# Kernel optimization log

Hardware: AMD Instinct MI355X
Metric: run time of the kernel (lower is better)

The kernel has to match this reference:

```python
import jax, jax.numpy as jnp
import numpy as np

B, S, F, H = 128, 1024, 512, 128


def setup_inputs() -> dict:
    key = jax.random.key(0)
    ks = jax.random.split(key, 12)
    # ragged valid lengths; force one full-length sequence so padded max == S
    lengths = jax.random.randint(ks[0], (B,), S // 4, S + 1)
    lengths = lengths.at[0].set(S)
    mask = (jnp.arange(S)[None, :] < lengths[:, None]).astype(jnp.float32)
    x = jax.random.normal(ks[1], (B, S, F), jnp.float32) * mask[:, :, None]
    s = 1.0 / np.sqrt(H)

    def u(k, shape):
        return jax.random.uniform(k, shape, jnp.float32, -s, s)

    return {
        "x": x,
        "Wp": u(ks[2], (H, F)), "bp": u(ks[3], (H,)),
        "Wih0": u(ks[4], (3 * H, H)), "Whh0": u(ks[5], (3 * H, H)),
        "bih0": u(ks[6], (3 * H,)), "bhh0": u(ks[7], (3 * H,)),
        "Wih1": u(ks[8], (3 * H, H)), "Whh1": u(ks[9], (3 * H, H)),
        "bih1": u(ks[10], (3 * H,)), "bhh1": u(ks[11], (3 * H,)),
    }


def _gru_layer(xs, Wih, Whh, bih, bhh):
    # xs: [S, B, H_in] -> outputs [S, B, H]; torch nn.GRU gate math (r,z,n order)
    xg = jnp.einsum('sbi,gi->sbg', xs, Wih) + bih  # precompute input gates [S,B,3H]
    Hh = Whh.shape[1]

    def step(h, xg_t):
        hg = h @ Whh.T + bhh
        xr, xz, xn = jnp.split(xg_t, 3, axis=-1)
        hr, hz, hn = jnp.split(hg, 3, axis=-1)
        r = jax.nn.sigmoid(xr + hr)
        z = jax.nn.sigmoid(xz + hz)
        n = jnp.tanh(xn + r * hn)
        h_new = (1.0 - z) * n + z * h
        return h_new, h_new

    h0 = jnp.zeros((xs.shape[1], Hh), xs.dtype)
    _, hs = jax.lax.scan(step, h0, xg)
    return hs


def reference(x, Wp, bp, Wih0, Whh0, bih0, bhh0, Wih1, Whh1, bih1, bhh1):
    # valid lengths: rows whose feature-sum is nonzero
    lengths = (jnp.sum(x, axis=-1) != 0).astype(jnp.int32).sum(axis=1)  # [B]
    proj = x @ Wp.T + bp  # [B,S,H]
    # sort by descending length (module returns outputs in SORTED order, no unsort)
    order = jnp.argsort(-lengths)
    sorted_lengths = lengths[order]
    xs = jnp.transpose(proj[order], (1, 0, 2))  # [S,B,H]
    h1 = _gru_layer(xs, Wih0, Whh0, bih0, bhh0)
    h2 = _gru_layer(h1, Wih1, Whh1, bih1, bhh1)
    out = jnp.transpose(h2, (1, 0, 2))  # [B,S,H]
    # pad_packed_sequence zeros outputs beyond each valid length
    valid = (jnp.arange(S)[None, :] < sorted_lengths[:, None]).astype(out.dtype)
    out = out * valid[:, :, None]
    # mean over padded length (max length == S here), zeros included, as in torch
    return out.mean(axis=1)
```

## Files before the change

### kernel.cpp

```cpp
#include <hip/hip_runtime.h>
#include <hip/hip_bf16.h>

#define BB 128
#define SS 1024
#define FF 512
#define HH 128
#define G3 384

typedef __attribute__((ext_vector_type(8))) short bf16x8;
typedef __attribute__((ext_vector_type(4))) float f32x4;
typedef _Float16 half2_t __attribute__((ext_vector_type(2)));

__global__ void zero_len_kernel(int* len) { len[threadIdx.x] = 0; }

__global__ void lengths_kernel(const float* __restrict__ x, int* __restrict__ len) {
    int wave = threadIdx.x >> 6;
    int lane = threadIdx.x & 63;
    long row = (long)blockIdx.x * 4 + wave;
    const float4* p = (const float4*)&x[row * FF + lane * 8];
    float4 v0 = p[0], v1 = p[1];
    float s = v0.x + v0.y + v0.z + v0.w + v1.x + v1.y + v1.z + v1.w;
    #pragma unroll
    for (int off = 32; off > 0; off >>= 1) s += __shfl_down(s, off, 64);
    if (lane == 0 && s != 0.0f) atomicAdd(&len[row >> 10], 1);
}

__global__ void rank_kernel(const int* __restrict__ len, int* __restrict__ rank) {
    int i = threadIdx.x;
    int li = len[i];
    int r = 0;
    for (int jj = 0; jj < BB; jj++) {
        int lj = len[jj];
        if (lj > li || (lj == li && jj < i)) r++;
    }
    rank[i] = r;
}

__device__ __forceinline__ short bf_hi(float w, float& hf) {
    unsigned u = __builtin_bit_cast(unsigned, w);
    unsigned r = (u + 0x7FFFu + ((u >> 16) & 1u)) & 0xFFFF0000u;
    hf = __builtin_bit_cast(float, r);
    return (short)(r >> 16);
}
__device__ __forceinline__ short bf_rn(float w) {
    unsigned u = __builtin_bit_cast(unsigned, w);
    unsigned r = u + 0x7FFFu + ((u >> 16) & 1u);
    return (short)(r >> 16);
}

__global__ __launch_bounds__(256) void gemm_mfma(
    const float* __restrict__ A, const float* __restrict__ W,
    const float* __restrict__ bias, float* __restrict__ C,
    int M, int N, int K)
{
    const int tid  = threadIdx.x;
    const int wvid = tid >> 6;
    const int lane = tid & 63;
    const int m0   = blockIdx.x * 64 + wvid * 16;
    const int n0   = blockIdx.y * 128;
    const int KS   = K >> 5;

    __shared__ __align__(16) short sh[2][8][64][8];

    f32x4 acc[8];
    #pragma unroll
    for (int i = 0; i < 8; i++) acc[i] = (f32x4){0.f, 0.f, 0.f, 0.f};

    const int arow = m0 + (lane & 15);
    const int koff = (lane >> 4) << 3;

    for (int ks = 0; ks < KS; ks++) {
        __syncthreads();
        #pragma unroll
        for (int i = 0; i < 2; i++) {
            int p  = tid + i * 256;
            int nt = p >> 6, ln = p & 63;
            const float* src = &W[(size_t)(n0 + nt * 16 + (ln & 15)) * K
                                  + ks * 32 + ((ln >> 4) << 3)];
            float w8[8];
            *(float4*)&w8[0] = *(const float4*)&src[0];
            *(float4*)&w8[4] = *(const float4*)&src[4];
            short hi8[8], lo8[8];
            #pragma unroll
            for (int e = 0; e < 8; e++) {
                float hf; hi8[e] = bf_hi(w8[e], hf);
                lo8[e] = bf_rn(w8[e] - hf);
            }
            *(bf16x8*)&sh[0][nt][ln][0] = *(bf16x8*)hi8;
            *(bf16x8*)&sh[1][nt][ln][0] = *(bf16x8*)lo8;
        }
        const float* ap = &A[(size_t)arow * K + ks * 32 + koff];
        float av[8];
        *(float4*)&av[0] = *(const float4*)&ap[0];
        *(float4*)&av[4] = *(const float4*)&ap[4];
        short ah[8], al[8];
        #pragma unroll
        for (int e = 0; e < 8; e++) {
            float hf; ah[e] = bf_hi(av[e], hf);
            al[e] = bf_rn(av[e] - hf);
        }
        bf16x8 ahi = *(bf16x8*)ah, alo = *(bf16x8*)al;
        __syncthreads();
        #pragma unroll
        for (int nt = 0; nt < 8; nt++) {
            bf16x8 bhi = *(bf16x8*)&sh[0][nt][lane][0];
            bf16x8 blo = *(bf16x8*)&sh[1][nt][lane][0];
            acc[nt] = __builtin_amdgcn_mfma_f32_16x16x32_bf16(ahi, bhi, acc[nt], 0, 0, 0);
            acc[nt] = __builtin_amdgcn_mfma_f32_16x16x32_bf16(ahi, blo, acc[nt], 0, 0, 0);
            acc[nt] = __builtin_amdgcn_mfma_f32_16x16x32_bf16(alo, bhi, acc[nt], 0, 0, 0);
        }
    }
    const int crow = m0 + ((lane >> 4) << 2);
    const int ccol = n0 + (lane & 15);
    #pragma unroll
    for (int nt = 0; nt < 8; nt++) {
        int col = ccol + nt * 16;
        float bv = bias[col];
        #pragma unroll
        for (int r = 0; r < 4; r++)
            C[(size_t)(crow + r) * N + col] = acc[nt][r] + bv;
    }
}

__device__ __forceinline__ float fast_sigmoid(float x) {
    return __builtin_amdgcn_rcpf(1.0f + __expf(-x));
}
__device__ __forceinline__ float fast_tanh(float x) {
    return 1.0f - 2.0f * __builtin_amdgcn_rcpf(1.0f + __expf(2.0f * x));
}
__device__ __forceinline__ half2_t bc16(unsigned u) {
    return __builtin_bit_cast(half2_t, u);
}
__device__ __forceinline__ unsigned pk16(float x, float y) {
    half2_t h; h[0] = (_Float16)x; h[1] = (_Float16)y;
    return __builtin_bit_cast(unsigned, h);
}
__device__ __forceinline__ float fdot2_(half2_t a, half2_t b, float c) {
#if __has_builtin(__builtin_amdgcn_fdot2)
    return __builtin_amdgcn_fdot2(a, b, c, false);
#else
    return c + (float)a[0] * (float)b[0] + (float)a[1] * (float)b[1];
#endif
}

template<int FINAL>
__global__ __launch_bounds__(512, 1) void gru_rec(
    const float* __restrict__ xg,
    const float* __restrict__ Whh,
    const float* __restrict__ bhh,
    float* __restrict__ h_out,
    const int* __restrict__ len,
    const int* __restrict__ rank)
{
    const int b   = blockIdx.x;
    const int tid = threadIdx.x;
    const int j   = tid >> 2;
    const int kq  = tid & 3;

    __shared__ __align__(16) _Float16 h16[2][HH];
    __shared__ __align__(16) float    h32[2][HH];

    unsigned wv[3][16];
    #pragma unroll
    for (int g = 0; g < 3; g++) {
        const float* wr = &Whh[(size_t)(g * HH + j) * HH + kq * 32];
        #pragma unroll
        for (int m = 0; m < 16; m++) wv[g][m] = pk16(wr[2 * m], wr[2 * m + 1]);
    }

    float b_r = 0.f, b_z = 0.f, b_n = 0.f;
    if (kq == 0) { b_r = bhh[j]; b_z = bhh[HH + j]; b_n = bhh[2 * HH + j]; }
    const float* xgb = xg + (size_t)b * SS * G3;

    if (tid < HH) { h16[0][tid] = (_Float16)0.f; h32[0][tid] = 0.f; }
    float hprev = 0.0f, osum = 0.0f;
    const int L = FINAL ? len[b] : 0;

    float xr = 0.f, xz = 0.f, xn = 0.f;
    if (kq == 0) { xr = xgb[j]; xz = xgb[HH + j]; xn = xgb[2 * HH + j]; }
    __syncthreads();

    for (int t = 0; t < SS; t++) {
        #pragma unroll
        for (int g = 0; g < 3; g++)
            #pragma unroll
            for (int m = 0; m < 16; m += 4)
                asm volatile("" : "+v"(wv[g][m]), "+v"(wv[g][m + 1]),
                                  "+v"(wv[g][m + 2]), "+v"(wv[g][m + 3]));

        if (!FINAL && t > 0 && tid >= 64 && tid < 96) {
            int c = tid - 64;
            float4 hv = ((const float4*)h32[t & 1])[c];
            *(float4*)&h_out[((size_t)b * SS + (t - 1)) * HH + c * 4] = hv;
        }
        float nxr = 0.f, nxz = 0.f, nxn = 0.f;
        if (kq == 0 && t + 1 < SS) {
            const float* p = xgb + (size_t)(t + 1) * G3;
            nxr = p[j]; nxz = p[HH + j]; nxn = p[2 * HH + j];
        }
        const unsigned* hp = (const unsigned*)(&h16[t & 1][0]) + kq * 16;
        float a0 = 0.f, a1 = 0.f, a2 = 0.f;
        float c0 = 0.f, c1 = 0.f, c2 = 0.f;
        #pragma unroll
        for (int i = 0; i < 4; i++) {
            uint4 hv = *(const uint4*)(hp + i * 4);
            half2_t q0 = bc16(hv.x), q1 = bc16(hv.y),
                    q2 = bc16(hv.z), q3 = bc16(hv.w);
            if ((i & 1) == 0) {
                a0 = fdot2_(bc16(wv[0][i * 4 + 0]), q0, a0);
                a0 = fdot2_(bc16(wv[0][i * 4 + 1]), q1, a0);
                a0 = fdot2_(bc16(wv[0][i * 4 + 2]), q2, a0);
                a0 = fdot2_(bc16(wv[0][i * 4 + 3]), q3, a0);
                a1 = fdot2_(bc16(wv[1][i * 4 + 0]), q0, a1);
                a1 = fdot2_(bc16(wv[1][i * 4 + 1]), q1, a1);
                a1 = fdot2_(bc16(wv[1][i * 4 + 2]), q2, a1);
                a1 = fdot2_(bc16(wv[1][i * 4 + 3]), q3, a1);
                a2 = fdot2_(bc16(wv[2][i * 4 + 0]), q0, a2);
                a2 = fdot2_(bc16(wv[2][i * 4 + 1]), q1, a2);
                a2 = fdot2_(bc16(wv[2][i * 4 + 2]), q2, a2);
                a2 = fdot2_(bc16(wv[2][i * 4 + 3]), q3, a2);
            } else {
                c0 = fdot2_(bc16(wv[0][i * 4 + 0]), q0, c0);
                c0 = fdot2_(bc16(wv[0][i * 4 + 1]), q1, c0);
                c0 = fdot2_(bc16(wv[0][i * 4 + 2]), q2, c0);
                c0 = fdot2_(bc16(wv[0][i * 4 + 3]), q3, c0);
                c1 = fdot2_(bc16(wv[1][i * 4 + 0]), q0, c1);
                c1 = fdot2_(bc16(wv[1][i * 4 + 1]), q1, c1);
                c1 = fdot2_(bc16(wv[1][i * 4 + 2]), q2, c1);
                c1 = fdot2_(bc16(wv[1][i * 4 + 3]), q3, c1);
                c2 = fdot2_(bc16(wv[2][i * 4 + 0]), q0, c2);
                c2 = fdot2_(bc16(wv[2][i * 4 + 1]), q1, c2);
                c2 = fdot2_(bc16(wv[2][i * 4 + 2]), q2, c2);
                c2 = fdot2_(bc16(wv[2][i * 4 + 3]), q3, c2);
            }
        }
        float s0 = a0 + c0, s1 = a1 + c1, s2 = a2 + c2;
        s0 += __shfl_xor(s0, 1, 64); s1 += __shfl_xor(s1, 1, 64); s2 += __shfl_xor(s2, 1, 64);
        s0 += __shfl_xor(s0, 2, 64); s1 += __shfl_xor(s1, 2, 64); s2 += __shfl_xor(s2, 2, 64);
        if (kq == 0) {
            float r = fast_sigmoid(xr + s0 + b_r);
            float z = fast_sigmoid(xz + s1 + b_z);
            float n = fast_tanh(xn + r * (s2 + b_n));
            float h = (1.0f - z) * n + z * hprev;
            hprev = h;
            h16[(t + 1) & 1][j] = (_Float16)h;
            h32[(t + 1) & 1][j] = h;
            if (FINAL) { if (t < L) osum += h; }
        }
        xr = nxr; xz = nxz; xn = nxn;
        __syncthreads();
    }
    if (!FINAL && tid >= 64 && tid < 96) {
        int c = tid - 64;
        float4 hv = ((const float4*)h32[SS & 1])[c];
        *(float4*)&h_out[((size_t)b * SS + (SS - 1)) * HH + c * 4] = hv;
    }
    if (FINAL && kq == 0) {
        h_out[(size_t)rank[b] * HH + j] = osum * (1.0f / (float)SS);
    }
}

extern "C" void kernel_launch(void* const* d_in, const int* in_sizes, int n_in,
                              void* d_out, int out_size, void* d_ws, size_t ws_size,
                              hipStream_t stream) {
    const float* x    = (const float*)d_in[0];
    const float* Wp   = (const float*)d_in[1];
    const float* bp   = (const float*)d_in[2];
    const float* Wih0 = (const float*)d_in[3];
    const float* Whh0 = (const float*)d_in[4];
    const float* bih0 = (const float*)d_in[5];
    const float* bhh0 = (const float*)d_in[6];
    const float* Wih1 = (const float*)d_in[7];
    const float* Whh1 = (const float*)d_in[8];
    const float* bih1 = (const float*)d_in[9];
    const float* bhh1 = (const float*)d_in[10];
    float* out = (float*)d_out;

    int* len  = (int*)d_ws;
    int* rank = len + 128;
    float* proj = (float*)((char*)d_ws + 4096);
    float* xgb  = proj + (size_t)BB * SS * HH;

    zero_len_kernel<<<1, 128, 0, stream>>>(len);
    lengths_kernel<<<(BB * SS) / 4, 256, 0, stream>>>(x, len);
    rank_kernel<<<1, 128, 0, stream>>>(len, rank);

    gemm_mfma<<<dim3(BB * SS / 64, 1), 256, 0, stream>>>(x, Wp, bp, proj,
                                                         BB * SS, HH, FF);
    gemm_mfma<<<dim3(BB * SS / 64, 3), 256, 0, stream>>>(proj, Wih0, bih0, xgb,
                                                         BB * SS, G3, HH);
    gru_rec<0><<<BB, 512, 0, stream>>>(xgb, Whh0, bhh0, proj, len, rank);

    gemm_mfma<<<dim3(BB * SS / 64, 3), 256, 0, stream>>>(proj, Wih1, bih1, xgb,
                                                         BB * SS, G3, HH);
    gru_rec<1><<<BB, 512, 0, stream>>>(xgb, Whh1, bhh1, out, len, rank);
}
```

Before: 2.058 ms.

## Store recurrent weights in AGPRs and reduce partial sums with DPP

Moves the 48 packed fp16 weight registers per thread out of VGPRs into accumulation registers, written once and read back with v_accvgpr_read before each dot product. The 4-lane partial-sum reduction now uses DPP quad permutes instead of ds_swizzle/shuffle, and the dot chain is reordered into two interleaved accumulators per gate. The goal is to relieve VGPR pressure and avoid spills at 512 threads per block, and to shorten the cross-lane reduction on the serial per-step path. In exchange, every step adds 48 AGPR read instructions, and the inline asm with hard-coded AGPR numbers may conflict with compiler register allocation.

```diff
diff --git a/kernel.cpp b/kernel.cpp
--- a/kernel.cpp
+++ b/kernel.cpp
@@ -142,6 +142,19 @@
     return c + (float)a[0] * (float)b[0] + (float)a[1] * (float)b[1];
 #endif
 }
+template<int CTRL>
+__device__ __forceinline__ float dpp_xor_add(float v) {
+    int vi = __builtin_bit_cast(int, v);
+    int sw = __builtin_amdgcn_update_dpp(0, vi, CTRL, 0xF, 0xF, true);
+    return v + __builtin_bit_cast(float, sw);
+}
+#define DPP_XOR1 0xB1
+#define DPP_XOR2 0x4E
+
+#define AW(N) asm volatile("v_accvgpr_write_b32 a" #N ", %0" :: "v"(wt[(N) & 15]) : "a" #N)
+#define DOT(N, ACC) do { unsigned _w; \
+    asm volatile("v_accvgpr_read_b32 %0, a" #N : "=v"(_w)); \
+    ACC = fdot2_(bc16(_w), bc16(hw[(N) & 15]), ACC); } while (0)
 
 template<int FINAL>
 __global__ __launch_bounds__(512, 1) void gru_rec(
@@ -160,13 +173,22 @@
     __shared__ __align__(16) _Float16 h16[2][HH];
     __shared__ __align__(16) float    h32[2][HH];
 
-    unsigned wv[3][16];
-    #pragma unroll
-    for (int g = 0; g < 3; g++) {
-        const float* wr = &Whh[(size_t)(g * HH + j) * HH + kq * 32];
-        #pragma unroll
-        for (int m = 0; m < 16; m++) wv[g][m] = pk16(wr[2 * m], wr[2 * m + 1]);
-    }
+    unsigned wt[16];
+    { const float* wr = &Whh[(size_t)(0 * HH + j) * HH + kq * 32];
+      #pragma unroll
+      for (int m = 0; m < 16; m++) wt[m] = pk16(wr[2*m], wr[2*m+1]); }
+    AW(0);  AW(1);  AW(2);  AW(3);  AW(4);  AW(5);  AW(6);  AW(7);
+    AW(8);  AW(9);  AW(10); AW(11); AW(12); AW(13); AW(14); AW(15);
+    { const float* wr = &Whh[(size_t)(1 * HH + j) * HH + kq * 32];
+      #pragma unroll
+      for (int m = 0; m < 16; m++) wt[m] = pk16(wr[2*m], wr[2*m+1]); }
+    AW(16); AW(17); AW(18); AW(19); AW(20); AW(21); AW(22); AW(23);
+    AW(24); AW(25); AW(26); AW(27); AW(28); AW(29); AW(30); AW(31);
+    { const float* wr = &Whh[(size_t)(2 * HH + j) * HH + kq * 32];
+      #pragma unroll
+      for (int m = 0; m < 16; m++) wt[m] = pk16(wr[2*m], wr[2*m+1]); }
+    AW(32); AW(33); AW(34); AW(35); AW(36); AW(37); AW(38); AW(39);
+    AW(40); AW(41); AW(42); AW(43); AW(44); AW(45); AW(46); AW(47);
 
     float b_r = 0.f, b_z = 0.f, b_n = 0.f;
     if (kq == 0) { b_r = bhh[j]; b_z = bhh[HH + j]; b_n = bhh[2 * HH + j]; }
@@ -181,16 +203,11 @@
     __syncthreads();
 
     for (int t = 0; t < SS; t++) {
-        #pragma unroll
-        for (int g = 0; g < 3; g++)
-            #pragma unroll
-            for (int m = 0; m < 16; m += 4)
-                asm volatile("" : "+v"(wv[g][m]), "+v"(wv[g][m + 1]),
-                                  "+v"(wv[g][m + 2]), "+v"(wv[g][m + 3]));
+        const int cb = t & 1, nb = (t + 1) & 1;
 
         if (!FINAL && t > 0 && tid >= 64 && tid < 96) {
             int c = tid - 64;
-            float4 hv = ((const float4*)h32[t & 1])[c];
+            float4 hv = ((const float4*)h32[cb])[c];
             *(float4*)&h_out[((size_t)b * SS + (t - 1)) * HH + c * 4] = hv;
         }
         float nxr = 0.f, nxz = 0.f, nxn = 0.f;
@@ -198,53 +215,43 @@
             const float* p = xgb + (size_t)(t + 1) * G3;
             nxr = p[j]; nxz = p[HH + j]; nxn = p[2 * HH + j];
         }
-        const unsigned* hp = (const unsigned*)(&h16[t & 1][0]) + kq * 16;
-        float a0 = 0.f, a1 = 0.f, a2 = 0.f;
-        float c0 = 0.f, c1 = 0.f, c2 = 0.f;
-        #pragma unroll
-        for (int i = 0; i < 4; i++) {
-            uint4 hv = *(const uint4*)(hp + i * 4);
-            half2_t q0 = bc16(hv.x), q1 = bc16(hv.y),
-                    q2 = bc16(hv.z), q3 = bc16(hv.w);
-            if ((i & 1) == 0) {
-                a0 = fdot2_(bc16(wv[0][i * 4 + 0]), q0, a0);
-                a0 = fdot2_(bc16(wv[0][i * 4 + 1]), q1, a0);
-                a0 = fdot2_(bc16(wv[0][i * 4 + 2]), q2, a0);
-                a0 = fdot2_(bc16(wv[0][i * 4 + 3]), q3, a0);
-                a1 = fdot2_(bc16(wv[1][i * 4 + 0]), q0, a1);
-                a1 = fdot2_(bc16(wv[1][i * 4 + 1]), q1, a1);
-                a1 = fdot2_(bc16(wv[1][i * 4 + 2]), q2, a1);
-                a1 = fdot2_(bc16(wv[1][i * 4 + 3]), q3, a1);
-                a2 = fdot2_(bc16(wv[2][i * 4 + 0]), q0, a2);
-                a2 = fdot2_(bc16(wv[2][i * 4 + 1]), q1, a2);
-                a2 = fdot2_(bc16(wv[2][i * 4 + 2]), q2, a2);
-                a2 = fdot2_(bc16(wv[2][i * 4 + 3]), q3, a2);
-            } else {
-                c0 = fdot2_(bc16(wv[0][i * 4 + 0]), q0, c0);
-                c0 = fdot2_(bc16(wv[0][i * 4 + 1]), q1, c0);
-                c0 = fdot2_(bc16(wv[0][i * 4 + 2]), q2, c0);
-                c0 = fdot2_(bc16(wv[0][i * 4 + 3]), q3, c0);
-                c1 = fdot2_(bc16(wv[1][i * 4 + 0]), q0, c1);
-                c1 = fdot2_(bc16(wv[1][i * 4 + 1]), q1, c1);
-                c1 = fdot2_(bc16(wv[1][i * 4 + 2]), q2, c1);
-                c1 = fdot2_(bc16(wv[1][i * 4 + 3]), q3, c1);
-                c2 = fdot2_(bc16(wv[2][i * 4 + 0]), q0, c2);
-                c2 = fdot2_(bc16(wv[2][i * 4 + 1]), q1, c2);
-                c2 = fdot2_(bc16(wv[2][i * 4 + 2]), q2, c2);
-                c2 = fdot2_(bc16(wv[2][i * 4 + 3]), q3, c2);
-            }
-        }
-        float s0 = a0 + c0, s1 = a1 + c1, s2 = a2 + c2;
-        s0 += __shfl_xor(s0, 1, 64); s1 += __shfl_xor(s1, 1, 64); s2 += __shfl_xor(s2, 1, 64);
-        s0 += __shfl_xor(s0, 2, 64); s1 += __shfl_xor(s1, 2, 64); s2 += __shfl_xor(s2, 2, 64);
+        const uint4* hp = (const uint4*)&h16[cb][kq * 32];
+        uint4 q0 = hp[0], q1 = hp[1], q2 = hp[2], q3 = hp[3];
+        unsigned hw[16] = {q0.x,q0.y,q0.z,q0.w, q1.x,q1.y,q1.z,q1.w,
+                           q2.x,q2.y,q2.z,q2.w, q3.x,q3.y,q3.z,q3.w};
+
+        float aA, aB;
+        aA = 0.f; aB = 0.f;
+        DOT(0,aA);  DOT(1,aB);  DOT(2,aA);  DOT(3,aB);
+        DOT(4,aA);  DOT(5,aB);  DOT(6,aA);  DOT(7,aB);
+        DOT(8,aA);  DOT(9,aB);  DOT(10,aA); DOT(11,aB);
+        DOT(12,aA); DOT(13,aB); DOT(14,aA); DOT(15,aB);
+        float s0 = aA + aB;
+        aA = 0.f; aB = 0.f;
+        DOT(16,aA); DOT(17,aB); DOT(18,aA); DOT(19,aB);
+        DOT(20,aA); DOT(21,aB); DOT(22,aA); DOT(23,aB);
+        DOT(24,aA); DOT(25,aB); DOT(26,aA); DOT(27,aB);
+        DOT(28,aA); DOT(29,aB); DOT(30,aA); DOT(31,aB);
+        float s1 = aA + aB;
+        aA = 0.f; aB = 0.f;
+        DOT(32,aA); DOT(33,aB); DOT(34,aA); DOT(35,aB);
+        DOT(36,aA); DOT(37,aB); DOT(38,aA); DOT(39,aB);
+        DOT(40,aA); DOT(41,aB); DOT(42,aA); DOT(43,aB);
+        DOT(44,aA); DOT(45,aB); DOT(46,aA); DOT(47,aB);
+        float s2 = aA + aB;
+
+        s0 = dpp_xor_add<DPP_XOR1>(s0); s0 = dpp_xor_add<DPP_XOR2>(s0);
+        s1 = dpp_xor_add<DPP_XOR1>(s1); s1 = dpp_xor_add<DPP_XOR2>(s1);
+        s2 = dpp_xor_add<DPP_XOR1>(s2); s2 = dpp_xor_add<DPP_XOR2>(s2);
+
         if (kq == 0) {
             float r = fast_sigmoid(xr + s0 + b_r);
             float z = fast_sigmoid(xz + s1 + b_z);
             float n = fast_tanh(xn + r * (s2 + b_n));
             float h = (1.0f - z) * n + z * hprev;
             hprev = h;
-            h16[(t + 1) & 1][j] = (_Float16)h;
-            h32[(t + 1) & 1][j] = h;
+            h16[nb][j] = (_Float16)h;
+            h32[nb][j] = h;
             if (FINAL) { if (t < L) osum += h; }
         }
         xr = nxr; xz = nxz; xn = nxn;
```

Result: slower. 2.188 ms (+6.3%).
